# Kernel tuning notes

Hardware: AMD Instinct MI355X
Metric: run time of the kernel (lower is better)

Reference implementation:

```python
import jax, jax.numpy as jnp
import numpy as np

H, DH, TXT, IMG_H, IMG_W = 24, 128, 512, 32, 32
HID, IPD, IPL, B = 3072, 1152, 128, 1
BBOX = (8, 8, 24, 24)  # x0, y0, x1, y1 in latent coords
IP_SCALE = 1.0


def _rms(x, w, eps=1e-6):
    return x * jax.lax.rsqrt(jnp.mean(x * x, axis=-1, keepdims=True) + eps) * w


def _lin(x, W, b):
    return x @ W.T + b


def _heads(x):
    b, l, d = x.shape
    return x.reshape(b, l, H, d // H).transpose(0, 2, 1, 3)  # [B,H,L,dh]


def _merge(x):
    b, h, l, d = x.shape
    return x.transpose(0, 2, 1, 3).reshape(b, l, h * d)


def _sdpa(q, k, v):
    s = jnp.einsum('bhqd,bhkd->bhqk', q, k) * (1.0 / np.sqrt(q.shape[-1]).astype(np.float32))
    return jnp.einsum('bhqk,bhkd->bhqd', jax.nn.softmax(s, axis=-1), v)


def _rope(x, cos, sin):
    # Flux real-valued rotary: interleaved pairs. x: [B,H,S,D], cos/sin: [S,D]
    xr = x.reshape(x.shape[:-1] + (-1, 2))
    x_rot = jnp.stack([-xr[..., 1], xr[..., 0]], axis=-1).reshape(x.shape)
    return x * cos + x_rot * sin


def reference(hidden_states, encoder_hidden_states, ip_hidden_states, rope_cos, rope_sin,
              Wq, bq, Wk, bk, Wv, bv, norm_q_w, norm_k_w,
              Wq_add, bq_add, Wk_add, bk_add, Wv_add, bv_add, norm_added_q_w, norm_added_k_w,
              W_out, b_out, W_add_out, b_add_out,
              W_k_ip, b_k_ip, W_v_ip, b_v_ip, norm_ip_q_w, norm_ip_k_w):
    q = _lin(hidden_states, Wq, bq)   # [B, IMG, HID] (image-stream tokens)
    k = _lin(hidden_states, Wk, bk)
    v = _lin(hidden_states, Wv, bv)

    # IP-adapter cross-attention: image query (pre norm_q / pre-RoPE) vs IP tokens
    ip_q = _rms(_heads(q), norm_ip_q_w)
    ip_k = _rms(_heads(_lin(ip_hidden_states, W_k_ip, b_k_ip)), norm_ip_k_w)
    ip_v = _heads(_lin(ip_hidden_states, W_v_ip, b_v_ip))
    ip_out = _merge(_sdpa(ip_q, ip_k, ip_v))  # [B, IMG, HID]

    qh = _rms(_heads(q), norm_q_w)
    kh = _rms(_heads(k), norm_k_w)
    vh = _heads(v)

    eq = _rms(_heads(_lin(encoder_hidden_states, Wq_add, bq_add)), norm_added_q_w)
    ek = _rms(_heads(_lin(encoder_hidden_states, Wk_add, bk_add)), norm_added_k_w)
    ev = _heads(_lin(encoder_hidden_states, Wv_add, bv_add))

    qf = _rope(jnp.concatenate([eq, qh], axis=2), rope_cos, rope_sin)
    kf = _rope(jnp.concatenate([ek, kh], axis=2), rope_cos, rope_sin)
    vf = jnp.concatenate([ev, vh], axis=2)

    out = _merge(_sdpa(qf, kf, vf))  # [B, TXT+IMG, HID]
    enc, img = out[:, :TXT], out[:, TXT:]

    # bbox mask over image tokens (static bbox -> static mask)
    mask = jnp.zeros((IMG_H, IMG_W), dtype=img.dtype)
    mask = mask.at[BBOX[1]:BBOX[3], BBOX[0]:BBOX[2]].set(1.0).reshape(-1)
    img = img + ip_out * (mask[None, :, None] * IP_SCALE)

    img = _lin(img, W_out, b_out)       # to_out[0]; to_out[1] is dropout(p=0)
    enc = _lin(enc, W_add_out, b_add_out)
    return img, enc


def setup_inputs() -> dict:
    key = jax.random.key(0)
    ks = iter(jax.random.split(key, 40))
    w = lambda shape, s=0.02: jax.random.normal(next(ks), shape, jnp.float32) * s
    S = TXT + IMG_H * IMG_W
    pos = jnp.arange(S, dtype=jnp.float32)
    freqs = 1.0 / (10000.0 ** (jnp.arange(0, DH, 2, dtype=jnp.float32) / DH))
    ang = jnp.repeat(pos[:, None] * freqs[None, :], 2, axis=-1)  # [S, DH]
    return dict(
        hidden_states=jax.random.normal(next(ks), (B, IMG_H * IMG_W, HID), jnp.float32),
        encoder_hidden_states=jax.random.normal(next(ks), (B, TXT, HID), jnp.float32),
        ip_hidden_states=jax.random.normal(next(ks), (B, IPL, IPD), jnp.float32),
        rope_cos=jnp.cos(ang), rope_sin=jnp.sin(ang),
        Wq=w((HID, HID)), bq=jnp.zeros((HID,), jnp.float32),
        Wk=w((HID, HID)), bk=jnp.zeros((HID,), jnp.float32),
        Wv=w((HID, HID)), bv=jnp.zeros((HID,), jnp.float32),
        norm_q_w=jnp.ones((DH,), jnp.float32), norm_k_w=jnp.ones((DH,), jnp.float32),
        Wq_add=w((HID, HID)), bq_add=jnp.zeros((HID,), jnp.float32),
        Wk_add=w((HID, HID)), bk_add=jnp.zeros((HID,), jnp.float32),
        Wv_add=w((HID, HID)), bv_add=jnp.zeros((HID,), jnp.float32),
        norm_added_q_w=jnp.ones((DH,), jnp.float32), norm_added_k_w=jnp.ones((DH,), jnp.float32),
        W_out=w((HID, HID)), b_out=jnp.zeros((HID,), jnp.float32),
        W_add_out=w((HID, HID)), b_add_out=jnp.zeros((HID,), jnp.float32),
        W_k_ip=w((HID, IPD)), b_k_ip=jnp.zeros((HID,), jnp.float32),
        W_v_ip=w((HID, IPD)), b_v_ip=jnp.zeros((HID,), jnp.float32),
        norm_ip_q_w=jnp.ones((DH,), jnp.float32), norm_ip_k_w=jnp.ones((DH,), jnp.float32),
    )
```

## Files before the change

### kernel.cpp

```cpp
#include <hip/hip_runtime.h>


#define HID 3072
#define DH 128
#define NH 24
#define TXT 512
#define SIMG 1024
#define SFULL 1536
#define IPL 128
#define IPD 1152
#define ATTN_SCALE 0.08838834764831845f

typedef unsigned short u16;
typedef __attribute__((ext_vector_type(8))) short bf16x8;
typedef __attribute__((ext_vector_type(4))) float f32x4;

#define LDST 40

__device__ __forceinline__ int xcd_swz(int flat, int nwg) {
  return (flat & 7) * (nwg >> 3) + (flat >> 3);
}

__device__ __forceinline__ unsigned pkbf(float a, float b) {
  unsigned r;
  asm("v_cvt_pk_bf16_f32 %0, %1, %2" : "=v"(r) : "v"(a), "v"(b));
  return r;
}

__device__ __forceinline__ void cvt_hi_lo(float4 fa, float4 fb, uint4* hi, uint4* lo) {
  unsigned h0 = pkbf(fa.x, fa.y), h1 = pkbf(fa.z, fa.w);
  unsigned h2 = pkbf(fb.x, fb.y), h3 = pkbf(fb.z, fb.w);
  float r0 = fa.x - __uint_as_float(h0 << 16);
  float r1 = fa.y - __uint_as_float(h0 & 0xffff0000u);
  float r2 = fa.z - __uint_as_float(h1 << 16);
  float r3 = fa.w - __uint_as_float(h1 & 0xffff0000u);
  float r4 = fb.x - __uint_as_float(h2 << 16);
  float r5 = fb.y - __uint_as_float(h2 & 0xffff0000u);
  float r6 = fb.z - __uint_as_float(h3 << 16);
  float r7 = fb.w - __uint_as_float(h3 & 0xffff0000u);
  *hi = make_uint4(h0, h1, h2, h3);
  *lo = make_uint4(pkbf(r0, r1), pkbf(r2, r3), pkbf(r4, r5), pkbf(r6, r7));
}

__device__ __forceinline__ void gemm128_core(
    const float* __restrict__ A, const float* __restrict__ W,
    const float* __restrict__ bias, float* __restrict__ C, int K, int ldC) {
  __shared__ short Ah[128 * LDST], Al[128 * LDST];
  __shared__ short Wh[128 * LDST], Wl[128 * LDST];
  const int tid = threadIdx.x;
  const int srow = tid >> 1;
  const int skb = (tid & 1) * 16;
  const int sidx = srow * LDST + skb;
  const int lane = tid & 63, w = tid >> 6;
  const int wm = (w >> 1) * 64, wn = (w & 1) * 64;
  const int fr = lane & 15, kg = lane >> 4;
  const int aoff = (wm + fr) * LDST + kg * 8;
  const int boff = (wn + fr) * LDST + kg * 8;
  const float* ap = A + (size_t)srow * K + skb;
  const float* wp = W + (size_t)srow * K + skb;

  f32x4 acc[4][4];
#pragma unroll
  for (int i = 0; i < 4; ++i)
#pragma unroll
    for (int j = 0; j < 4; ++j) acc[i][j] = (f32x4){0.f, 0.f, 0.f, 0.f};

  for (int k0 = 0; k0 < K; k0 += 32) {
    float4 a0 = *(const float4*)(ap + k0);
    float4 a1 = *(const float4*)(ap + k0 + 4);
    float4 a2 = *(const float4*)(ap + k0 + 8);
    float4 a3 = *(const float4*)(ap + k0 + 12);
    float4 b0 = *(const float4*)(wp + k0);
    float4 b1 = *(const float4*)(wp + k0 + 4);
    float4 b2 = *(const float4*)(wp + k0 + 8);
    float4 b3 = *(const float4*)(wp + k0 + 12);
    uint4 h, l;
    cvt_hi_lo(a0, a1, &h, &l);
    *(uint4*)&Ah[sidx] = h;     *(uint4*)&Al[sidx] = l;
    cvt_hi_lo(a2, a3, &h, &l);
    *(uint4*)&Ah[sidx + 8] = h; *(uint4*)&Al[sidx + 8] = l;
    cvt_hi_lo(b0, b1, &h, &l);
    *(uint4*)&Wh[sidx] = h;     *(uint4*)&Wl[sidx] = l;
    cvt_hi_lo(b2, b3, &h, &l);
    *(uint4*)&Wh[sidx + 8] = h; *(uint4*)&Wl[sidx + 8] = l;
    __syncthreads();
    bf16x8 fah[4], fal[4], fbh[4], fbl[4];
#pragma unroll
    for (int f = 0; f < 4; ++f) {
      fah[f] = *(const bf16x8*)&Ah[aoff + f * 16 * LDST];
      fal[f] = *(const bf16x8*)&Al[aoff + f * 16 * LDST];
      fbh[f] = *(const bf16x8*)&Wh[boff + f * 16 * LDST];
      fbl[f] = *(const bf16x8*)&Wl[boff + f * 16 * LDST];
    }
#pragma unroll
    for (int fm = 0; fm < 4; ++fm)
#pragma unroll
      for (int fn = 0; fn < 4; ++fn) {
        acc[fm][fn] = __builtin_amdgcn_mfma_f32_16x16x32_bf16(fah[fm], fbh[fn], acc[fm][fn], 0, 0, 0);
        acc[fm][fn] = __builtin_amdgcn_mfma_f32_16x16x32_bf16(fal[fm], fbh[fn], acc[fm][fn], 0, 0, 0);
        acc[fm][fn] = __builtin_amdgcn_mfma_f32_16x16x32_bf16(fah[fm], fbl[fn], acc[fm][fn], 0, 0, 0);
      }
    __syncthreads();
  }
  const int r4 = kg * 4;
#pragma unroll
  for (int fn = 0; fn < 4; ++fn) {
    float bb = bias[wn + fn * 16 + fr];
#pragma unroll
    for (int fm = 0; fm < 4; ++fm) {
      f32x4 v = acc[fm][fn];
#pragma unroll
      for (int j = 0; j < 4; ++j)
        C[(size_t)(wm + fm * 16 + r4 + j) * ldC + (wn + fn * 16 + fr)] = v[j] + bb;
    }
  }
}

struct Seg3 {
  const float *W0, *W1, *W2;
  const float *b0, *b1, *b2;
  float *C0, *C1, *C2;
};

__global__ __launch_bounds__(256) void gemm_seg3(const float* __restrict__ A, Seg3 s, int K) {
  const int nwg = gridDim.x * gridDim.y;
  const int sw = xcd_swz(blockIdx.y * gridDim.x + blockIdx.x, nwg);
  const int by = sw % gridDim.y;
  const int bx = sw / gridDim.y;
  const int seg = bx / 24;
  const int n0 = (bx % 24) * 128;
  const int m0 = by * 128;
  const float* W = seg == 0 ? s.W0 : (seg == 1 ? s.W1 : s.W2);
  const float* b = seg == 0 ? s.b0 : (seg == 1 ? s.b1 : s.b2);
  float* C = seg == 0 ? s.C0 : (seg == 1 ? s.C1 : s.C2);
  gemm128_core(A + (size_t)m0 * K, W + (size_t)n0 * K, b + n0,
               C + (size_t)m0 * HID + n0, K, HID);
}

__global__ __launch_bounds__(256) void gemm_out2(
    const float* __restrict__ A,
    const float* __restrict__ We, const float* __restrict__ be, float* __restrict__ Ce,
    const float* __restrict__ Wi, const float* __restrict__ bi, float* __restrict__ Ci,
    int K) {
  const int nwg = gridDim.x * gridDim.y;
  const int sw = xcd_swz(blockIdx.y * gridDim.x + blockIdx.x, nwg);
  const int by = sw % gridDim.y;
  const int bx = sw / gridDim.y;
  const int m0 = by * 128;
  const int n0 = bx * 128;
  const float* W; const float* b; float* C; int cr;
  if (m0 < TXT) { W = We; b = be; C = Ce; cr = m0; }
  else          { W = Wi; b = bi; C = Ci; cr = m0 - TXT; }
  gemm128_core(A + (size_t)m0 * K, W + (size_t)n0 * K, b + n0,
               C + (size_t)cr * HID + n0, K, HID);
}

__device__ __forceinline__ float blk_sum128(float v, float* red) {
  int d = threadIdx.x;
  red[d] = v; __syncthreads();
  if (d < 64) red[d] += red[d + 64]; __syncthreads();
  if (d < 32) red[d] += red[d + 32]; __syncthreads();
  if (d < 16) red[d] += red[d + 16]; __syncthreads();
  if (d < 8)  red[d] += red[d + 8];  __syncthreads();
  if (d < 4)  red[d] += red[d + 4];  __syncthreads();
  if (d < 2)  red[d] += red[d + 2];  __syncthreads();
  if (d < 1)  red[d] += red[d + 1];  __syncthreads();
  float r = red[0]; __syncthreads();
  return r;
}
__device__ __forceinline__ float blk_max128(float v, float* red) {
  int d = threadIdx.x;
  red[d] = v; __syncthreads();
  if (d < 64) red[d] = fmaxf(red[d], red[d + 64]); __syncthreads();
  if (d < 32) red[d] = fmaxf(red[d], red[d + 32]); __syncthreads();
  if (d < 16) red[d] = fmaxf(red[d], red[d + 16]); __syncthreads();
  if (d < 8)  red[d] = fmaxf(red[d], red[d + 8]);  __syncthreads();
  if (d < 4)  red[d] = fmaxf(red[d], red[d + 4]);  __syncthreads();
  if (d < 2)  red[d] = fmaxf(red[d], red[d + 2]);  __syncthreads();
  if (d < 1)  red[d] = fmaxf(red[d], red[d + 1]);  __syncthreads();
  float r = red[0]; __syncthreads();
  return r;
}

__global__ __launch_bounds__(128) void ip_norm_reorder(
    const float* __restrict__ src, const float* __restrict__ w,
    float* __restrict__ dst, int do_norm) {
  __shared__ float red[128];
  const int t = blockIdx.x, h = blockIdx.y, d = threadIdx.x;
  float v = src[(size_t)t * HID + h * DH + d];
  if (do_norm) {
    float ss = blk_sum128(v * v, red);
    v = v * rsqrtf(ss * (1.0f / DH) + 1e-6f) * w[d];
  }
  dst[((size_t)h * IPL + t) * DH + d] = v;
}

__global__ __launch_bounds__(128) void ip_attn(
    const float* __restrict__ Q, const float* __restrict__ KN,
    const float* __restrict__ VN, const float* __restrict__ qw,
    float* __restrict__ OUTc) {
  const int b = blockIdx.x, h = blockIdx.y, d = threadIdx.x;
  const int y = 8 + (b >> 4), x = 8 + (b & 15);
  const int t = y * 32 + x;
  __shared__ float qs[128], ps[128], red[128];
  float qv = Q[(size_t)t * HID + h * DH + d];
  float ss = blk_sum128(qv * qv, red);
  qs[d] = qv * rsqrtf(ss * (1.0f / DH) + 1e-6f) * qw[d];
  __syncthreads();
  const float* krow = KN + ((size_t)h * IPL + d) * DH;
  float s = 0.f;
#pragma unroll 4
  for (int i = 0; i < 128; ++i) s += qs[i] * krow[i];
  s *= ATTN_SCALE;
  float mx = blk_max128(s, red);
  float p = __expf(s - mx);
  ps[d] = p;
  float lsum = blk_sum128(p, red);
  const float* vcol = VN + (size_t)h * IPL * DH + d;
  float o = 0.f;
#pragma unroll 4
  for (int j = 0; j < 128; ++j) o += ps[j] * vcol[(size_t)j * DH];
  OUTc[(size_t)b * HID + h * DH + d] = o / lsum;
}

__global__ __launch_bounds__(768) void rmsrope_cvt(
    float* __restrict__ img, float* __restrict__ enc,
    const float* __restrict__ w_img, const float* __restrict__ w_enc,
    const float* __restrict__ cosb, const float* __restrict__ sinb, float scale) {
  const int s = blockIdx.x;
  const int t = threadIdx.x;
  float* row = (s < TXT) ? (enc + (size_t)s * HID) : (img + (size_t)(s - TXT) * HID);
  const float* w = (s < TXT) ? w_enc : w_img;
  const int dh = (t & 31) * 4;
  float4 v = *(const float4*)(row + t * 4);
  float ss = v.x * v.x + v.y * v.y + v.z * v.z + v.w * v.w;
  ss += __shfl_xor(ss, 16); ss += __shfl_xor(ss, 8);
  ss += __shfl_xor(ss, 4);  ss += __shfl_xor(ss, 2); ss += __shfl_xor(ss, 1);
  float r = rsqrtf(ss * (1.0f / DH) + 1e-6f);
  float4 wv = *(const float4*)(w + dh);
  float n0 = v.x * r * wv.x, n1 = v.y * r * wv.y;
  float n2 = v.z * r * wv.z, n3 = v.w * r * wv.w;
  float4 cv = *(const float4*)(cosb + (size_t)s * DH + dh);
  float4 sv = *(const float4*)(sinb + (size_t)s * DH + dh);
  float o0 = (n0 * cv.x - n1 * sv.x) * scale;
  float o1 = (n1 * cv.y + n0 * sv.y) * scale;
  float o2 = (n2 * cv.z - n3 * sv.z) * scale;
  float o3 = (n3 * cv.w + n2 * sv.w) * scale;
  __syncthreads();
  unsigned h0 = pkbf(o0, o1), h1 = pkbf(o2, o3);
  float l0 = o0 - __uint_as_float(h0 << 16);
  float l1 = o1 - __uint_as_float(h0 & 0xffff0000u);
  float l2 = o2 - __uint_as_float(h1 << 16);
  float l3 = o3 - __uint_as_float(h1 & 0xffff0000u);
  unsigned lw0 = pkbf(l0, l1), lw1 = pkbf(l2, l3);
  unsigned* ur = (unsigned*)row;
  *(uint2*)(ur + t * 2) = make_uint2(h0, h1);
  *(uint2*)(ur + 1536 + t * 2) = make_uint2(lw0, lw1);
}

__global__ __launch_bounds__(256) void v_cvt_transpose(
    const float* __restrict__ Vimg, const float* __restrict__ Venc,
    u16* __restrict__ VTh, u16* __restrict__ VTl) {
  __shared__ float T[64][132];
  const int kc = blockIdx.x, h = blockIdx.y, tid = threadIdx.x;
  {
    const int r = tid >> 2, c = tid & 3;
    const int kk = kc * 64 + r;
    const float* src = ((kk < TXT) ? (Venc + (size_t)kk * HID)
                                   : (Vimg + (size_t)(kk - TXT) * HID)) + h * DH + c * 32;
#pragma unroll
    for (int i = 0; i < 8; ++i)
      *(float4*)&T[r][c * 32 + i * 4] = *(const float4*)(src + i * 4);
  }
  __syncthreads();
  const int d = tid >> 1, kh = tid & 1;
  unsigned hw[16], lw[16];
#pragma unroll
  for (int i = 0; i < 16; ++i) {
    float a = T[kh * 32 + i * 2 + 0][d];
    float b = T[kh * 32 + i * 2 + 1][d];
    unsigned hh = pkbf(a, b);
    float la = a - __uint_as_float(hh << 16);
    float lb = b - __uint_as_float(hh & 0xffff0000u);
    hw[i] = hh; lw[i] = pkbf(la, lb);
  }
  size_t base = ((size_t)h * DH + d) * SFULL + kc * 64 + kh * 32;
#pragma unroll
  for (int i = 0; i < 4; ++i) {
    *(uint4*)(VTh + base + i * 8) = make_uint4(hw[i*4], hw[i*4+1], hw[i*4+2], hw[i*4+3]);
    *(uint4*)(VTl + base + i * 8) = make_uint4(lw[i*4], lw[i*4+1], lw[i*4+2], lw[i*4+3]);
  }
}

#define KVB 32
#define NKT (SFULL / KVB)

__global__ __launch_bounds__(256, 3) void flash_mfma(
    const float* __restrict__ Qimg, const float* __restrict__ Qenc,
    const float* __restrict__ Kimg, const float* __restrict__ Kenc,
    const u16* __restrict__ VTh, const u16* __restrict__ VTl,
    const float* __restrict__ IPOc, float* __restrict__ AOUT) {
  __shared__ __align__(16) u16 Klds[2][KVB * 128];
  __shared__ __align__(16) u16 Vlds[2][128 * 40];
  __shared__ __align__(16) u16 Plds[4][2][16 * 40];
  const int tid = threadIdx.x;
  const int lane = tid & 63, w = tid >> 6;
  const int sw = xcd_swz(blockIdx.y * gridDim.x + blockIdx.x, 24 * NH);
  const int h = sw / 24;
  const int q0 = (sw % 24) * 64;
  const int l15 = lane & 15, lg = lane >> 4;

  bf16x8 qf[4][2];
  {
    const int qrow = q0 + w * 16 + l15;
    const u16* rp = (qrow < TXT) ? (const u16*)(Qenc + (size_t)qrow * HID)
                                 : (const u16*)(Qimg + (size_t)(qrow - TXT) * HID);
#pragma unroll
    for (int ks = 0; ks < 4; ++ks) {
      qf[ks][0] = *(const bf16x8*)(rp + h * DH + ks * 32 + lg * 8);
      qf[ks][1] = *(const bf16x8*)(rp + 3072 + h * DH + ks * 32 + lg * 8);
    }
  }

  f32x4 O[8];
#pragma unroll
  for (int i = 0; i < 8; ++i) O[i] = (f32x4){0.f, 0.f, 0.f, 0.f};
  float mrun[4], lrun[4];
#pragma unroll
  for (int j = 0; j < 4; ++j) { mrun[j] = -1e30f; lrun[j] = 0.f; }

  uint4 kr[4], vr[4];
#define STAGE_LOAD(kt)                                                          \
  {                                                                             \
    _Pragma("unroll")                                                           \
    for (int it = 0; it < 4; ++it) {                                            \
      const int c = tid + it * 256;                                             \
      const int pl = c >> 9, rowk = (c >> 4) & 31, ch = c & 15;                 \
      const int kk = (kt) * KVB + rowk;                                         \
      const u16* rp = (kk < TXT) ? (const u16*)(Kenc + (size_t)kk * HID)        \
                                 : (const u16*)(Kimg + (size_t)(kk - TXT) * HID); \
      kr[it] = *(const uint4*)(rp + pl * 3072 + h * DH + ch * 8);               \
      const int dv = (c >> 2) & 127, cv = c & 3;                                \
      const u16* vp = (pl ? VTl : VTh) + ((size_t)h * DH + dv) * SFULL          \
                      + (kt) * KVB + cv * 8;                                    \
      vr[it] = *(const uint4*)vp;                                               \
    }                                                                           \
  }

  STAGE_LOAD(0)
  for (int kt = 0; kt < NKT; ++kt) {
    __syncthreads();
#pragma unroll
    for (int it = 0; it < 4; ++it) {
      const int c = tid + it * 256;
      const int pl = c >> 9, rowk = (c >> 4) & 31, ch = c & 15;
      *(uint4*)((char*)&Klds[pl][0] + ((rowk * 256 + ch * 16) ^ ((rowk & 7) << 4))) = kr[it];
      const int dv = (c >> 2) & 127, cv = c & 3;
      *(uint4*)&Vlds[pl][dv * 40 + cv * 8] = vr[it];
    }
    const int ktn = (kt + 1 < NKT) ? kt + 1 : kt;
    STAGE_LOAD(ktn)
    __syncthreads();

    f32x4 sA[2] = {(f32x4){0.f, 0.f, 0.f, 0.f}, (f32x4){0.f, 0.f, 0.f, 0.f}};
#pragma unroll
    for (int ks = 0; ks < 4; ++ks)
#pragma unroll
      for (int fn = 0; fn < 2; ++fn) {
        const int krow = fn * 16 + l15;
        const int off = (krow * 256 + ks * 64 + lg * 16) ^ ((krow & 7) << 4);
        bf16x8 kh = *(const bf16x8*)((const char*)&Klds[0][0] + off);
        bf16x8 kl = *(const bf16x8*)((const char*)&Klds[1][0] + off);
        sA[fn] = __builtin_amdgcn_mfma_f32_16x16x32_bf16(qf[ks][0], kh, sA[fn], 0, 0, 0);
        sA[fn] = __builtin_amdgcn_mfma_f32_16x16x32_bf16(qf[ks][1], kh, sA[fn], 0, 0, 0);
        sA[fn] = __builtin_amdgcn_mfma_f32_16x16x32_bf16(qf[ks][0], kl, sA[fn], 0, 0, 0);
      }

#pragma unroll
    for (int j = 0; j < 4; ++j) {
      float v0 = sA[0][j], v1 = sA[1][j];
      float mx = fmaxf(v0, v1);
      mx = fmaxf(mx, __shfl_xor(mx, 1));
      mx = fmaxf(mx, __shfl_xor(mx, 2));
      mx = fmaxf(mx, __shfl_xor(mx, 4));
      mx = fmaxf(mx, __shfl_xor(mx, 8));
      float mnew = fmaxf(mrun[j], mx);
      float a = __expf(mrun[j] - mnew);
      mrun[j] = mnew;
      float p0 = __expf(v0 - mnew), p1 = __expf(v1 - mnew);
      float ts = p0 + p1;
      ts += __shfl_xor(ts, 1); ts += __shfl_xor(ts, 2);
      ts += __shfl_xor(ts, 4); ts += __shfl_xor(ts, 8);
      lrun[j] = lrun[j] * a + ts;
#pragma unroll
      for (int fn = 0; fn < 8; ++fn) O[fn][j] *= a;
      unsigned hp0 = pkbf(p0, 0.f), hp1 = pkbf(p1, 0.f);
      float lp0 = p0 - __uint_as_float(hp0 << 16);
      float lp1 = p1 - __uint_as_float(hp1 << 16);
      unsigned lo0 = pkbf(lp0, 0.f), lo1 = pkbf(lp1, 0.f);
      const int q = lg * 4 + j;
      Plds[w][0][q * 40 + l15]      = (u16)hp0;
      Plds[w][0][q * 40 + 16 + l15] = (u16)hp1;
      Plds[w][1][q * 40 + l15]      = (u16)lo0;
      Plds[w][1][q * 40 + 16 + l15] = (u16)lo1;
    }

    bf16x8 pa0 = *(const bf16x8*)&Plds[w][0][l15 * 40 + lg * 8];
    bf16x8 pa1 = *(const bf16x8*)&Plds[w][1][l15 * 40 + lg * 8];
#pragma unroll
    for (int fn = 0; fn < 8; ++fn) {
      const int dd = fn * 16 + l15;
      bf16x8 vh = *(const bf16x8*)&Vlds[0][dd * 40 + lg * 8];
      bf16x8 vl = *(const bf16x8*)&Vlds[1][dd * 40 + lg * 8];
      O[fn] = __builtin_amdgcn_mfma_f32_16x16x32_bf16(pa0, vh, O[fn], 0, 0, 0);
      O[fn] = __builtin_amdgcn_mfma_f32_16x16x32_bf16(pa1, vh, O[fn], 0, 0, 0);
      O[fn] = __builtin_amdgcn_mfma_f32_16x16x32_bf16(pa0, vl, O[fn], 0, 0, 0);
    }
  }
#undef STAGE_LOAD

#pragma unroll
  for (int j = 0; j < 4; ++j) {
    const float inv = 1.0f / lrun[j];
    const int s = q0 + w * 16 + lg * 4 + j;
    float* orow = AOUT + (size_t)s * HID + h * DH;
    const float* iprow = nullptr;
    if (s >= TXT) {
      const int t2 = s - TXT, y = t2 >> 5, x = t2 & 31;
      if (y >= 8 && y < 24 && x >= 8 && x < 24)
        iprow = IPOc + (size_t)((y - 8) * 16 + (x - 8)) * HID + h * DH;
    }
#pragma unroll
    for (int fn = 0; fn < 8; ++fn) {
      float val = O[fn][j] * inv;
      const int dd = fn * 16 + l15;
      if (iprow) val += iprow[dd];
      orow[dd] = val;
    }
  }
}

extern "C" void kernel_launch(void* const* d_in, const int* in_sizes, int n_in,
                              void* d_out, int out_size, void* d_ws, size_t ws_size,
                              hipStream_t stream) {
  const float* x    = (const float*)d_in[0];
  const float* enc  = (const float*)d_in[1];
  const float* ip   = (const float*)d_in[2];
  const float* cosb = (const float*)d_in[3];
  const float* sinb = (const float*)d_in[4];
  const float* Wq   = (const float*)d_in[5];
  const float* bq   = (const float*)d_in[6];
  const float* Wk   = (const float*)d_in[7];
  const float* bk   = (const float*)d_in[8];
  const float* Wv   = (const float*)d_in[9];
  const float* bv   = (const float*)d_in[10];
  const float* nqw  = (const float*)d_in[11];
  const float* nkw  = (const float*)d_in[12];
  const float* Wqa  = (const float*)d_in[13];
  const float* bqa  = (const float*)d_in[14];
  const float* Wka  = (const float*)d_in[15];
  const float* bka  = (const float*)d_in[16];
  const float* Wva  = (const float*)d_in[17];
  const float* bva  = (const float*)d_in[18];
  const float* naqw = (const float*)d_in[19];
  const float* nakw = (const float*)d_in[20];
  const float* Wo   = (const float*)d_in[21];
  const float* bo   = (const float*)d_in[22];
  const float* Wao  = (const float*)d_in[23];
  const float* bao  = (const float*)d_in[24];
  const float* Wkip = (const float*)d_in[25];
  const float* bkip = (const float*)d_in[26];
  const float* Wvip = (const float*)d_in[27];
  const float* bvip = (const float*)d_in[28];
  const float* nipq = (const float*)d_in[29];
  const float* nipk = (const float*)d_in[30];

  float* out_img = (float*)d_out;
  float* out_enc = (float*)d_out + (size_t)SIMG * HID;

  float* ws = (float*)d_ws;
  float* Qi  = ws + 0;
  float* Qe  = ws + 3145728;
  float* Ki  = ws + 4718592;
  float* Ke  = ws + 7864320;
  float* Vi  = ws + 9437184;
  float* Ve  = ws + 12582912;
  float* VTr = ws + 14155776;
  float* IPOc= ws + 18874368;
  float* KIP  = VTr;
  float* VIP  = VTr + 393216;
  float* KIPN = VTr + 786432;
  float* VIPN = VTr + 1179648;
  u16* VTh = (u16*)VTr;
  u16* VTl = (u16*)(VTr + 2359296);
  float* AOUT = Vi;

  dim3 blk256(256), blk128(128);

  gemm_seg3<<<dim3(72, 8), blk256, 0, stream>>>(
      x, Seg3{Wq, Wk, Wv, bq, bk, bv, Qi, Ki, Vi}, HID);
  gemm_seg3<<<dim3(72, 4), blk256, 0, stream>>>(
      enc, Seg3{Wqa, Wka, Wva, bqa, bka, bva, Qe, Ke, Ve}, HID);
  gemm_seg3<<<dim3(48, 1), blk256, 0, stream>>>(
      ip, Seg3{Wkip, Wvip, Wvip, bkip, bvip, bvip, KIP, VIP, VIP}, IPD);
  ip_norm_reorder<<<dim3(IPL, NH), blk128, 0, stream>>>(KIP, nipk, KIPN, 1);
  ip_norm_reorder<<<dim3(IPL, NH), blk128, 0, stream>>>(VIP, nullptr, VIPN, 0);
  ip_attn<<<dim3(256, NH), blk128, 0, stream>>>(Qi, KIPN, VIPN, nipq, IPOc);
  rmsrope_cvt<<<dim3(SFULL), dim3(768), 0, stream>>>(Qi, Qe, nqw, naqw, cosb, sinb, ATTN_SCALE);
  rmsrope_cvt<<<dim3(SFULL), dim3(768), 0, stream>>>(Ki, Ke, nkw, nakw, cosb, sinb, 1.0f);
  v_cvt_transpose<<<dim3(24, NH), blk256, 0, stream>>>(Vi, Ve, VTh, VTl);
  flash_mfma<<<dim3(24, NH), blk256, 0, stream>>>(Qi, Qe, Ki, Ke, VTh, VTl, IPOc, AOUT);
  gemm_out2<<<dim3(24, 12), blk256, 0, stream>>>(
      AOUT, Wao, bao, out_enc, Wo, bo, out_img, HID);
}
```

Before: 1.494 ms.

## Stream K/V tiles into double-buffered LDS with direct global-to-LDS loads

```diff
diff --git a/kernel.cpp b/kernel.cpp
--- a/kernel.cpp
+++ b/kernel.cpp
@@ -19,6 +19,12 @@
 
 __device__ __forceinline__ int xcd_swz(int flat, int nwg) {
   return (flat & 7) * (nwg >> 3) + (flat >> 3);
+}
+
+__device__ __forceinline__ void gload16(const void* src, void* dst) {
+  __builtin_amdgcn_global_load_lds(
+      (const __attribute__((address_space(1))) void*)(void*)src,
+      (__attribute__((address_space(3))) void*)dst, 16, 0, 0);
 }
 
 __device__ __forceinline__ unsigned pkbf(float a, float b) {
@@ -295,14 +301,13 @@
 #define KVB 32
 #define NKT (SFULL / KVB)
 
-__global__ __launch_bounds__(256, 3) void flash_mfma(
+__global__ __launch_bounds__(256) void flash_mfma(
     const float* __restrict__ Qimg, const float* __restrict__ Qenc,
     const float* __restrict__ Kimg, const float* __restrict__ Kenc,
     const u16* __restrict__ VTh, const u16* __restrict__ VTl,
     const float* __restrict__ IPOc, float* __restrict__ AOUT) {
-  __shared__ __align__(16) u16 Klds[2][KVB * 128];
-  __shared__ __align__(16) u16 Vlds[2][128 * 40];
-  __shared__ __align__(16) u16 Plds[4][2][16 * 40];
+  __shared__ __align__(16) u16 Stage[2][18432];
+  __shared__ __align__(16) u16 Plds[4][2][16 * 32];
   const int tid = threadIdx.x;
   const int lane = tid & 63, w = tid >> 6;
   const int sw = xcd_swz(blockIdx.y * gridDim.x + blockIdx.x, 24 * NH);
@@ -329,38 +334,42 @@
 #pragma unroll
   for (int j = 0; j < 4; ++j) { mrun[j] = -1e30f; lrun[j] = 0.f; }
 
-  uint4 kr[4], vr[4];
-#define STAGE_LOAD(kt)                                                          \
-  {                                                                             \
-    _Pragma("unroll")                                                           \
-    for (int it = 0; it < 4; ++it) {                                            \
-      const int c = tid + it * 256;                                             \
-      const int pl = c >> 9, rowk = (c >> 4) & 31, ch = c & 15;                 \
-      const int kk = (kt) * KVB + rowk;                                         \
-      const u16* rp = (kk < TXT) ? (const u16*)(Kenc + (size_t)kk * HID)        \
-                                 : (const u16*)(Kimg + (size_t)(kk - TXT) * HID); \
-      kr[it] = *(const uint4*)(rp + pl * 3072 + h * DH + ch * 8);               \
-      const int dv = (c >> 2) & 127, cv = c & 3;                                \
-      const u16* vp = (pl ? VTl : VTh) + ((size_t)h * DH + dv) * SFULL          \
-                      + (kt) * KVB + cv * 8;                                    \
-      vr[it] = *(const uint4*)vp;                                               \
-    }                                                                           \
-  }
-
-  STAGE_LOAD(0)
+  auto stage_issue = [&](int kt, u16* dstbase) {
+    const int kr0 = kt * KVB;
+    const float* kb = (kr0 < TXT) ? Kenc : Kimg;
+    const int kro = (kr0 < TXT) ? 0 : TXT;
+#pragma unroll
+    for (int i = 0; i < 9; ++i) {
+      const int c = w * 9 + i;
+      u16* dst = dstbase + c * 512;
+      const u16* src;
+      if (c < 16) {
+        const int plane = c >> 3;
+        const int po = (c & 7) * 1024 + lane * 16;
+        const int rowk = po >> 8;
+        const int ch = ((po >> 4) & 15) ^ (rowk & 7);
+        src = (const u16*)(kb + (size_t)(kr0 + rowk - kro) * HID)
+              + plane * HID + h * DH + ch * 8;
+      } else {
+        const int plane = (c >= 26) ? 1 : 0;
+        const int t16 = ((c - (plane ? 26 : 16)) * 1024 + lane * 16) >> 4;
+        const int dv = (t16 * 52429) >> 18;
+        int part = t16 - dv * 5; part = (part > 3) ? 3 : part;
+        src = (plane ? VTl : VTh) + ((size_t)(h * DH + dv)) * SFULL
+              + kr0 + part * 8;
+      }
+      gload16(src, dst);
+    }
+  };
+
+  stage_issue(0, &Stage[0][0]);
+  asm volatile("s_waitcnt vmcnt(0)" ::: "memory");
+  __builtin_amdgcn_s_barrier();
+  __builtin_amdgcn_sched_barrier(0);
+
   for (int kt = 0; kt < NKT; ++kt) {
-    __syncthreads();
-#pragma unroll
-    for (int it = 0; it < 4; ++it) {
-      const int c = tid + it * 256;
-      const int pl = c >> 9, rowk = (c >> 4) & 31, ch = c & 15;
-      *(uint4*)((char*)&Klds[pl][0] + ((rowk * 256 + ch * 16) ^ ((rowk & 7) << 4))) = kr[it];
-      const int dv = (c >> 2) & 127, cv = c & 3;
-      *(uint4*)&Vlds[pl][dv * 40 + cv * 8] = vr[it];
-    }
-    const int ktn = (kt + 1 < NKT) ? kt + 1 : kt;
-    STAGE_LOAD(ktn)
-    __syncthreads();
+    u16* SB = &Stage[kt & 1][0];
+    if (kt + 1 < NKT) stage_issue(kt + 1, &Stage[(kt + 1) & 1][0]);
 
     f32x4 sA[2] = {(f32x4){0.f, 0.f, 0.f, 0.f}, (f32x4){0.f, 0.f, 0.f, 0.f}};
 #pragma unroll
@@ -369,8 +378,8 @@
       for (int fn = 0; fn < 2; ++fn) {
         const int krow = fn * 16 + l15;
         const int off = (krow * 256 + ks * 64 + lg * 16) ^ ((krow & 7) << 4);
-        bf16x8 kh = *(const bf16x8*)((const char*)&Klds[0][0] + off);
-        bf16x8 kl = *(const bf16x8*)((const char*)&Klds[1][0] + off);
+        bf16x8 kh = *(const bf16x8*)((const char*)SB + off);
+        bf16x8 kl = *(const bf16x8*)((const char*)SB + 8192 + off);
         sA[fn] = __builtin_amdgcn_mfma_f32_16x16x32_bf16(qf[ks][0], kh, sA[fn], 0, 0, 0);
         sA[fn] = __builtin_amdgcn_mfma_f32_16x16x32_bf16(qf[ks][1], kh, sA[fn], 0, 0, 0);
         sA[fn] = __builtin_amdgcn_mfma_f32_16x16x32_bf16(qf[ks][0], kl, sA[fn], 0, 0, 0);
@@ -399,25 +408,31 @@
       float lp1 = p1 - __uint_as_float(hp1 << 16);
       unsigned lo0 = pkbf(lp0, 0.f), lo1 = pkbf(lp1, 0.f);
       const int q = lg * 4 + j;
-      Plds[w][0][q * 40 + l15]      = (u16)hp0;
-      Plds[w][0][q * 40 + 16 + l15] = (u16)hp1;
-      Plds[w][1][q * 40 + l15]      = (u16)lo0;
-      Plds[w][1][q * 40 + 16 + l15] = (u16)lo1;
-    }
-
-    bf16x8 pa0 = *(const bf16x8*)&Plds[w][0][l15 * 40 + lg * 8];
-    bf16x8 pa1 = *(const bf16x8*)&Plds[w][1][l15 * 40 + lg * 8];
+      Plds[w][0][q * 32 + l15]      = (u16)hp0;
+      Plds[w][0][q * 32 + 16 + l15] = (u16)hp1;
+      Plds[w][1][q * 32 + l15]      = (u16)lo0;
+      Plds[w][1][q * 32 + 16 + l15] = (u16)lo1;
+    }
+
+    bf16x8 pa0 = *(const bf16x8*)&Plds[w][0][l15 * 32 + lg * 8];
+    bf16x8 pa1 = *(const bf16x8*)&Plds[w][1][l15 * 32 + lg * 8];
+    const u16* VhB = SB + 8192;
+    const u16* VlB = SB + 13312;
 #pragma unroll
     for (int fn = 0; fn < 8; ++fn) {
       const int dd = fn * 16 + l15;
-      bf16x8 vh = *(const bf16x8*)&Vlds[0][dd * 40 + lg * 8];
-      bf16x8 vl = *(const bf16x8*)&Vlds[1][dd * 40 + lg * 8];
+      bf16x8 vh = *(const bf16x8*)(VhB + dd * 40 + lg * 8);
+      bf16x8 vl = *(const bf16x8*)(VlB + dd * 40 + lg * 8);
       O[fn] = __builtin_amdgcn_mfma_f32_16x16x32_bf16(pa0, vh, O[fn], 0, 0, 0);
       O[fn] = __builtin_amdgcn_mfma_f32_16x16x32_bf16(pa1, vh, O[fn], 0, 0, 0);
       O[fn] = __builtin_amdgcn_mfma_f32_16x16x32_bf16(pa0, vl, O[fn], 0, 0, 0);
     }
-  }
-#undef STAGE_LOAD
+
+    __builtin_amdgcn_sched_barrier(0);
+    asm volatile("s_waitcnt vmcnt(0)" ::: "memory");
+    __builtin_amdgcn_s_barrier();
+    __builtin_amdgcn_sched_barrier(0);
+  }
 
 #pragma unroll
   for (int j = 0; j < 4; ++j) {
```

Result: faster. 1.402 ms (-6.1%).
